# Kernel optimization log

Measured on AMD Instinct MI355X. Metric: run time of the kernel, lower is better.

Reference implementation:

```python
import jax, jax.numpy as jnp
import numpy as np

S, B, E, H, DFF = 1024, 8, 1024, 16, 4096
D = E // H
EPS = 1e-5


def _layernorm(x, g, b):
    m = jnp.mean(x, axis=-1, keepdims=True)
    v = jnp.mean(jnp.square(x - m), axis=-1, keepdims=True)
    return (x - m) * jax.lax.rsqrt(v + EPS) * g + b


def setup_inputs() -> dict:
    key = jax.random.key(0)
    ks = jax.random.split(key, 6)
    return {
        "src": jax.random.normal(ks[0], (S, B, E), jnp.float32),
        "in_proj_w": jax.random.normal(ks[1], (3 * E, E), jnp.float32) * (E ** -0.5),
        "in_proj_b": jnp.zeros((3 * E,), jnp.float32),
        "out_w": jax.random.normal(ks[2], (E, E), jnp.float32) * (E ** -0.5),
        "out_b": jnp.zeros((E,), jnp.float32),
        "ln1_g": jnp.ones((E,), jnp.float32),
        "ln1_b": jnp.zeros((E,), jnp.float32),
        "ln2_g": jnp.ones((E,), jnp.float32),
        "ln2_b": jnp.zeros((E,), jnp.float32),
        "w1": jax.random.normal(ks[3], (DFF, E), jnp.float32) * (E ** -0.5),
        "b1": jnp.zeros((DFF,), jnp.float32),
        "w2": jax.random.normal(ks[4], (E, DFF), jnp.float32) * (DFF ** -0.5),
        "b2": jnp.zeros((E,), jnp.float32),
    }


def reference(src, in_proj_w, in_proj_b, out_w, out_b, ln1_g, ln1_b, ln2_g, ln2_b, w1, b1, w2, b2):
    # src: (S, B, E). Packed in-projection: qkv = src @ W^T + b, split into q,k,v.
    qkv = src @ in_proj_w.T + in_proj_b          # (S, B, 3E)
    q, k, v = jnp.split(qkv, 3, axis=-1)
    q = q.reshape(S, B, H, D)
    k = k.reshape(S, B, H, D)
    v = v.reshape(S, B, H, D)
    # Torch scales q by 1/sqrt(head_dim) before the bmm.
    scores = jnp.einsum("sbhd,tbhd->bhst", q * (D ** -0.5), k)   # (B, H, S, S)
    attn = jax.nn.softmax(scores, axis=-1)
    ctx = jnp.einsum("bhst,tbhd->sbhd", attn, v).reshape(S, B, E)
    attn_out = ctx @ out_w.T + out_b
    # Post-norm encoder layer (norm_first=False), dropout=0.
    x = _layernorm(src + attn_out, ln1_g, ln1_b)
    ff = jax.nn.relu(x @ w1.T + b1) @ w2.T + b2
    return _layernorm(x + ff, ln2_g, ln2_b)
```

## Files before the change

kernel.cpp:

```cpp
#include <hip/hip_runtime.h>

#define S_LEN 1024
#define BATCH 8
#define EMB   1024
#define NH    16
#define HD    64
#define FFD   4096
#define ROWS  (S_LEN*BATCH)

typedef __attribute__((ext_vector_type(8))) short  short8;
typedef __attribute__((ext_vector_type(4))) float  float4v;
typedef __attribute__((ext_vector_type(4))) unsigned int uint4v;

struct alignas(8) us4 { unsigned short x, y, z, w; };

__device__ __forceinline__ unsigned short f2bf(float f) {
    unsigned int u = __float_as_uint(f);
    u += 0x7fffu + ((u >> 16) & 1u);
    return (unsigned short)(u >> 16);
}
__device__ __forceinline__ float bf2f(unsigned short b) {
    return __uint_as_float((unsigned int)b << 16);
}
__device__ __forceinline__ unsigned int cvtpk_bf16(float lo, float hi) {
    unsigned int r;
    asm("v_cvt_pk_bf16_f32 %0, %1, %2" : "=v"(r) : "v"(lo), "v"(hi));
    return r;
}
__device__ __forceinline__ float exp2v(float x) {
    float r;
    asm("v_exp_f32 %0, %1" : "=v"(r) : "v"(x));
    return r;
}

__device__ __forceinline__ void gload_lds16(const void* g, void* l) {
    __builtin_amdgcn_global_load_lds(
        (const __attribute__((address_space(1))) unsigned int*)g,
        (__attribute__((address_space(3))) unsigned int*)l, 16, 0, 0);
}

__device__ __forceinline__ int swz(int row, int chunk) {
    return (row << 7) + ((chunk ^ (row & 7)) << 4);
}

__device__ __forceinline__ void xcd_decode(int id, int& lx, int& ly) {
    int k = id & 7, j = id >> 3;
    ly = k * 4 + (j & 3);
    lx = j >> 2;
}

__global__ __launch_bounds__(256) void cast_bf(const float* __restrict__ in,
                                               unsigned short* __restrict__ out,
                                               int n4) {
    int i = blockIdx.x * 256 + threadIdx.x;
    if (i >= n4) return;
    float4 v = ((const float4*)in)[i];
    us4 o = { f2bf(v.x), f2bf(v.y), f2bf(v.z), f2bf(v.w) };
    ((us4*)out)[i] = o;
}

#define QSCALE 0.18033688011112042f
template <int MODE>
__global__ __launch_bounds__(512, 2) void gemm256(const unsigned short* __restrict__ A,
                                                  const unsigned short* __restrict__ Bw,
                                                  const float* __restrict__ bias,
                                                  unsigned short* __restrict__ outb,
                                                  int M, int N, int K) {
    __shared__ char lds[131072];
    const int tid = threadIdx.x, lane = tid & 63, w = tid >> 6;
    const int wr = w >> 2, wc = w & 3;
    int lx, ly;
    xcd_decode(blockIdx.x, lx, ly);
    const int m0 = ly * 256, n0 = lx * 256;
    const int nt = K >> 6;

    size_t baseA[2], baseB[2];
    int ldsOff[2];
#pragma unroll
    for (int q = 0; q < 2; ++q) {
        int ci = q * 512 + tid;
        int row = ci >> 3;
        int c = (ci & 7) ^ (row & 7);
        baseA[q] = (size_t)(m0 + row) * K + c * 8;
        baseB[q] = (size_t)(n0 + row) * K + c * 8;
        ldsOff[q] = ci * 16;
    }

    auto stage = [&](int kt, int which) {
        int ktc = kt < nt ? kt : 0;
        int slot = kt & 1;
        if (which < 2) {
#pragma unroll
            for (int q = 0; q < 2; ++q)
                gload_lds16(A + baseA[q] + (size_t)which * 128 * K + (size_t)ktc * 64,
                            lds + slot * 32768 + which * 16384 + ldsOff[q]);
        } else {
            int h = which - 2;
#pragma unroll
            for (int q = 0; q < 2; ++q)
                gload_lds16(Bw + baseB[q] + (size_t)h * 128 * K + (size_t)ktc * 64,
                            lds + 65536 + slot * 32768 + h * 16384 + ldsOff[q]);
        }
    };

    auto rdA = [&](int slot, int mh, int i, int mk) -> short8 {
        int arow = wr * 128 + mh * 64 + i * 16 + (lane & 15);
        return *(const short8*)(lds + slot * 32768 + swz(arow, mk * 4 + (lane >> 4)));
    };
    auto rdB = [&](int slot, int nh, int j, int mk) -> short8 {
        int brow = wc * 64 + nh * 32 + j * 16 + (lane & 15);
        return *(const short8*)(lds + 65536 + slot * 32768 + swz(brow, mk * 4 + (lane >> 4)));
    };

    float4v acc[8][4];
#pragma unroll
    for (int i = 0; i < 8; ++i)
#pragma unroll
        for (int j = 0; j < 4; ++j) acc[i][j] = (float4v){0.f, 0.f, 0.f, 0.f};

    short8 a[4][2], b[2][2][2];

    stage(0, 0); stage(0, 1); stage(0, 2); stage(0, 3);
    stage(1, 0);
    asm volatile("s_waitcnt vmcnt(2)" ::: "memory");
    __builtin_amdgcn_s_barrier();

#define MFMA16(MH, NH)                                                          \
    __builtin_amdgcn_s_setprio(1);                                              \
    _Pragma("unroll")                                                           \
    for (int i = 0; i < 4; ++i)                                                 \
        _Pragma("unroll")                                                       \
        for (int j = 0; j < 2; ++j) {                                           \
            acc[(MH)*4+i][(NH)*2+j] = __builtin_amdgcn_mfma_f32_16x16x32_bf16(  \
                a[i][0], b[NH][j][0], acc[(MH)*4+i][(NH)*2+j], 0, 0, 0);        \
            acc[(MH)*4+i][(NH)*2+j] = __builtin_amdgcn_mfma_f32_16x16x32_bf16(  \
                a[i][1], b[NH][j][1], acc[(MH)*4+i][(NH)*2+j], 0, 0, 0);        \
        }                                                                       \
    __builtin_amdgcn_s_setprio(0);

    for (int t = 0; t < nt; ++t) {
        const int slot = t & 1;
#pragma unroll
        for (int i = 0; i < 4; ++i) {
            a[i][0] = rdA(slot, 0, i, 0);
            a[i][1] = rdA(slot, 0, i, 1);
        }
#pragma unroll
        for (int j = 0; j < 2; ++j) {
            b[0][j][0] = rdB(slot, 0, j, 0);
            b[0][j][1] = rdB(slot, 0, j, 1);
        }
        stage(t + 1, 1);
        __builtin_amdgcn_s_barrier();
        asm volatile("s_waitcnt lgkmcnt(0)" ::: "memory");
        __builtin_amdgcn_sched_barrier(0);
        MFMA16(0, 0)
        __builtin_amdgcn_s_barrier();
#pragma unroll
        for (int j = 0; j < 2; ++j) {
            b[1][j][0] = rdB(slot, 1, j, 0);
            b[1][j][1] = rdB(slot, 1, j, 1);
        }
        stage(t + 1, 2);
        __builtin_amdgcn_s_barrier();
        asm volatile("s_waitcnt lgkmcnt(0)" ::: "memory");
        __builtin_amdgcn_sched_barrier(0);
        MFMA16(0, 1)
        __builtin_amdgcn_s_barrier();
#pragma unroll
        for (int i = 0; i < 4; ++i) {
            a[i][0] = rdA(slot, 1, i, 0);
            a[i][1] = rdA(slot, 1, i, 1);
        }
        stage(t + 1, 3);
        __builtin_amdgcn_s_barrier();
        asm volatile("s_waitcnt lgkmcnt(0)" ::: "memory");
        __builtin_amdgcn_sched_barrier(0);
        MFMA16(1, 1)
        __builtin_amdgcn_s_barrier();
        stage(t + 2, 0);
        MFMA16(1, 0)
        asm volatile("s_waitcnt vmcnt(2)" ::: "memory");
        __builtin_amdgcn_s_barrier();
    }
#undef MFMA16
    asm volatile("s_waitcnt vmcnt(0)" ::: "memory");

#pragma unroll
    for (int mi = 0; mi < 8; ++mi) {
#pragma unroll
        for (int nj = 0; nj < 4; ++nj) {
            int col = n0 + wc * 64 + nj * 16 + (lane & 15);
            float bv = bias[col];
#pragma unroll
            for (int r = 0; r < 4; ++r) {
                int row = m0 + wr * 128 + mi * 16 + (lane >> 4) * 4 + r;
                size_t idx = (size_t)row * N + col;
                float v = acc[mi][nj][r] + bv;
                if (MODE == 0) {
                    if (col < EMB) v *= QSCALE;
                    outb[idx] = f2bf(v);
                } else {
                    outb[idx] = f2bf(fmaxf(v, 0.f));
                }
            }
        }
    }
}

template <int MODE>
__global__ __launch_bounds__(512, 2) void gemm256n(const unsigned short* __restrict__ A,
                                                   const unsigned short* __restrict__ Bw,
                                                   const float* __restrict__ bias,
                                                   const float* __restrict__ res,
                                                   const unsigned short* __restrict__ resb,
                                                   float* __restrict__ outf,
                                                   int M, int N, int K) {
    __shared__ char lds[98304];
    const int tid = threadIdx.x, lane = tid & 63, w = tid >> 6;
    const int wr = w >> 1, wc = w & 1;
    int lx, ly;
    xcd_decode(blockIdx.x, lx, ly);
    const int m0 = ly * 256, n0 = lx * 128;
    const int nt = K >> 6;
    const int g = lane >> 4, qs = lane & 15;

    size_t baseA[4], baseB[2];
    int ldsOffA[4], ldsOffB[2];
#pragma unroll
    for (int q = 0; q < 4; ++q) {
        int ci = q * 512 + tid;
        int row = ci >> 3;
        int c = (ci & 7) ^ (row & 7);
        baseA[q] = (size_t)(m0 + row) * K + c * 8;
        ldsOffA[q] = ci * 16;
    }
#pragma unroll
    for (int q = 0; q < 2; ++q) {
        int ci = q * 512 + tid;
        int row = ci >> 3;
        int c = (ci & 7) ^ (row & 7);
        baseB[q] = (size_t)(n0 + row) * K + c * 8;
        ldsOffB[q] = ci * 16;
    }

    auto stage = [&](int kt, int which) {
        int ktc = kt < nt ? kt : 0;
        int slot = kt & 1;
        if (which < 2) {
#pragma unroll
            for (int q = 0; q < 2; ++q) {
                int qq = which * 2 + q;
                gload_lds16(A + baseA[qq] + (size_t)ktc * 64,
                            lds + slot * 32768 + ldsOffA[qq]);
            }
        } else {
#pragma unroll
            for (int q = 0; q < 2; ++q)
                gload_lds16(Bw + baseB[q] + (size_t)ktc * 64,
                            lds + 65536 + slot * 16384 + ldsOffB[q]);
        }
    };

    auto rdA = [&](int slot, int i, int mk) -> short8 {
        int arow = wr * 64 + i * 16 + qs;
        return *(const short8*)(lds + slot * 32768 + swz(arow, mk * 4 + g));
    };
    auto rdB = [&](int slot, int j, int mk) -> short8 {
        int brow = wc * 64 + j * 16 + qs;
        return *(const short8*)(lds + 65536 + slot * 16384 + swz(brow, mk * 4 + g));
    };

    float4v acc[4][4];
#pragma unroll
    for (int i = 0; i < 4; ++i)
#pragma unroll
        for (int j = 0; j < 4; ++j) acc[i][j] = (float4v){0.f, 0.f, 0.f, 0.f};

    short8 a[4][2], b[4][2];

    stage(0, 0); stage(0, 1); stage(0, 2);
    stage(1, 0);
    asm volatile("s_waitcnt vmcnt(2)" ::: "memory");
    __builtin_amdgcn_s_barrier();

    for (int t = 0; t < nt; ++t) {
        const int slot = t & 1;
#pragma unroll
        for (int i = 0; i < 4; ++i) {
            a[i][0] = rdA(slot, i, 0);
            a[i][1] = rdA(slot, i, 1);
        }
#pragma unroll
        for (int j = 0; j < 2; ++j) {
            b[j][0] = rdB(slot, j, 0);
            b[j][1] = rdB(slot, j, 1);
        }
        stage(t + 1, 1);
        __builtin_amdgcn_s_barrier();
        asm volatile("s_waitcnt lgkmcnt(0)" ::: "memory");
        __builtin_amdgcn_sched_barrier(0);
        __builtin_amdgcn_s_setprio(1);
#pragma unroll
        for (int i = 0; i < 4; ++i)
#pragma unroll
            for (int j = 0; j < 2; ++j) {
                acc[i][j] = __builtin_amdgcn_mfma_f32_16x16x32_bf16(
                    a[i][0], b[j][0], acc[i][j], 0, 0, 0);
                acc[i][j] = __builtin_amdgcn_mfma_f32_16x16x32_bf16(
                    a[i][1], b[j][1], acc[i][j], 0, 0, 0);
            }
        __builtin_amdgcn_s_setprio(0);
        __builtin_amdgcn_s_barrier();
#pragma unroll
        for (int j = 2; j < 4; ++j) {
            b[j][0] = rdB(slot, j, 0);
            b[j][1] = rdB(slot, j, 1);
        }
        stage(t + 1, 2);
        __builtin_amdgcn_s_barrier();
        asm volatile("s_waitcnt lgkmcnt(0)" ::: "memory");
        __builtin_amdgcn_sched_barrier(0);
        __builtin_amdgcn_s_setprio(1);
#pragma unroll
        for (int i = 0; i < 4; ++i)
#pragma unroll
            for (int j = 2; j < 4; ++j)
                acc[i][j] = __builtin_amdgcn_mfma_f32_16x16x32_bf16(
                    a[i][0], b[j][0], acc[i][j], 0, 0, 0);
        __builtin_amdgcn_s_setprio(0);
        __builtin_amdgcn_s_barrier();
        stage(t + 2, 0);
        __builtin_amdgcn_s_setprio(1);
#pragma unroll
        for (int i = 0; i < 4; ++i)
#pragma unroll
            for (int j = 2; j < 4; ++j)
                acc[i][j] = __builtin_amdgcn_mfma_f32_16x16x32_bf16(
                    a[i][1], b[j][1], acc[i][j], 0, 0, 0);
        __builtin_amdgcn_s_setprio(0);
        asm volatile("s_waitcnt vmcnt(2)" ::: "memory");
        __builtin_amdgcn_s_barrier();
    }
    asm volatile("s_waitcnt vmcnt(0)" ::: "memory");

#pragma unroll
    for (int mi = 0; mi < 4; ++mi) {
#pragma unroll
        for (int j = 0; j < 4; ++j) {
            int col = n0 + wc * 64 + j * 16 + qs;
            float bv = bias[col];
#pragma unroll
            for (int r = 0; r < 4; ++r) {
                int row = m0 + wr * 64 + mi * 16 + g * 4 + r;
                size_t idx = (size_t)row * N + col;
                float v = acc[mi][j][r] + bv;
                if (MODE == 1) outf[idx] = v + res[idx];
                else           outf[idx] = v + bf2f(resb[idx]);
            }
        }
    }
}

__global__ __launch_bounds__(256) void vtrans(const unsigned short* __restrict__ qkv,
                                              unsigned short* __restrict__ vt) {
    const int bh = blockIdx.y, b = bh >> 4, h = bh & 15;
    const int t0 = blockIdx.x * 64;
    const int tid = threadIdx.x;
    __shared__ unsigned short lds[64][72];
#pragma unroll
    for (int rep = 0; rep < 2; ++rep) {
        int slot = rep * 256 + tid;
        int row = slot >> 3, cc = slot & 7;
        const unsigned short* g =
            qkv + ((size_t)(t0 + row) * BATCH + b) * 3072 + 2 * EMB + h * 64 + cc * 8;
        *(uint4v*)&lds[row][cc * 8] = *(const uint4v*)g;
    }
    __syncthreads();
#pragma unroll
    for (int rep = 0; rep < 2; ++rep) {
        int slot = rep * 256 + tid;
        int d = slot >> 3, tc = slot & 7;
        unsigned short tmp[8] __attribute__((aligned(16)));
#pragma unroll
        for (int j = 0; j < 8; ++j) tmp[j] = lds[tc * 8 + j][d];
        unsigned short* g = vt + ((size_t)bh * 64 + d) * S_LEN + t0 + tc * 8;
        *(uint4v*)g = *(const uint4v*)tmp;
    }
}

__global__ __launch_bounds__(256, 6) void attn(const unsigned short* __restrict__ qkv,
                                               const unsigned short* __restrict__ vt,
                                               unsigned short* __restrict__ ctx) {
    __shared__ char Ks[64 * 128];
    __shared__ char Vs[64 * 128];
    __shared__ char QP[64 * 128];
    const int tid = threadIdx.x, lane = tid & 63, w = tid >> 6;
    const int bh = blockIdx.x & 127, b = bh >> 4, h = bh & 15;
    const int s0 = (blockIdx.x >> 7) * 64;
    const int g = lane >> 4, qs = lane & 15;

#pragma unroll
    for (int p = 0; p < 2; ++p) {
        int ci = p * 256 + tid;
        int row = ci >> 3, c = (ci & 7) ^ (row & 7);
        gload_lds16(qkv + ((size_t)(s0 + row) * BATCH + b) * 3072 + h * 64 + c * 8,
                    QP + (p * 256 + w * 64) * 16);
    }
    __syncthreads();

    short8 qa0 = *(const short8*)(QP + swz(w * 16 + qs, 0 * 4 + g));
    short8 qa1 = *(const short8*)(QP + swz(w * 16 + qs, 1 * 4 + g));
    asm volatile("s_waitcnt lgkmcnt(0)" ::: "memory");
    __builtin_amdgcn_sched_barrier(0);
    char* Ps = QP + w * 2048;

    float4v O[4];
#pragma unroll
    for (int df = 0; df < 4; ++df) O[df] = (float4v){0.f, 0.f, 0.f, 0.f};
    float m_s = -1e30f;
    float l_s = 0.f;

    for (int t0 = 0; t0 < S_LEN; t0 += 64) {
        __syncthreads();
#pragma unroll
        for (int p = 0; p < 2; ++p) {
            int ci = p * 256 + tid;
            int row = ci >> 3, c = (ci & 7) ^ (row & 7);
            gload_lds16(qkv + ((size_t)(t0 + row) * BATCH + b) * 3072 + EMB + h * 64 + c * 8,
                        Ks + (p * 256 + w * 64) * 16);
            gload_lds16(vt + ((size_t)bh * 64 + row) * S_LEN + t0 + c * 8,
                        Vs + (p * 256 + w * 64) * 16);
        }
        __syncthreads();

        float4v Sf[4];
#pragma unroll
        for (int tf = 0; tf < 4; ++tf) Sf[tf] = (float4v){0.f, 0.f, 0.f, 0.f};
#pragma unroll
        for (int tf = 0; tf < 4; ++tf) {
            int kr = tf * 16 + qs;
            short8 kb0 = *(const short8*)(Ks + swz(kr, 0 * 4 + g));
            short8 kb1 = *(const short8*)(Ks + swz(kr, 1 * 4 + g));
            Sf[tf] = __builtin_amdgcn_mfma_f32_16x16x32_bf16(kb0, qa0, Sf[tf], 0, 0, 0);
            Sf[tf] = __builtin_amdgcn_mfma_f32_16x16x32_bf16(kb1, qa1, Sf[tf], 0, 0, 0);
        }

        float mx = fmaxf(fmaxf(Sf[0][0], Sf[0][1]), fmaxf(Sf[0][2], Sf[0][3]));
#pragma unroll
        for (int tf = 1; tf < 4; ++tf)
            mx = fmaxf(mx, fmaxf(fmaxf(Sf[tf][0], Sf[tf][1]),
                                 fmaxf(Sf[tf][2], Sf[tf][3])));
        mx = fmaxf(mx, __shfl_xor(mx, 16));
        mx = fmaxf(mx, __shfl_xor(mx, 32));

        if (!__all(mx - m_s <= 8.0f)) {
            float mnew = fmaxf(m_s, mx);
            float alpha = exp2v(m_s - mnew);
            m_s = mnew;
            l_s *= alpha;
#pragma unroll
            for (int r = 0; r < 4; ++r) {
                float ar = __shfl(alpha, 4 * g + r);
#pragma unroll
                for (int df = 0; df < 4; ++df) O[df][r] *= ar;
            }
        }

        float rs = 0.f;
#pragma unroll
        for (int tf = 0; tf < 4; ++tf) {
            float p0 = exp2v(Sf[tf][0] - m_s);
            float p1 = exp2v(Sf[tf][1] - m_s);
            float p2 = exp2v(Sf[tf][2] - m_s);
            float p3 = exp2v(Sf[tf][3] - m_s);
            rs += (p0 + p1) + (p2 + p3);
            uint2 pk = make_uint2(cvtpk_bf16(p0, p1), cvtpk_bf16(p2, p3));
            *(uint2*)(Ps + (qs << 7) +
                      (((2 * tf + (g >> 1)) ^ (qs & 7)) << 4) + ((g & 1) << 3)) = pk;
        }
        rs += __shfl_xor(rs, 16);
        rs += __shfl_xor(rs, 32);
        l_s += rs;

        asm volatile("s_waitcnt lgkmcnt(0)" ::: "memory");
        __builtin_amdgcn_sched_barrier(0);

#pragma unroll
        for (int mk = 0; mk < 2; ++mk) {
            short8 pa = *(const short8*)(Ps + swz(qs, mk * 4 + g));
#pragma unroll
            for (int df = 0; df < 4; ++df) {
                int vr = df * 16 + qs;
                short8 vb = *(const short8*)(Vs + swz(vr, mk * 4 + g));
                O[df] = __builtin_amdgcn_mfma_f32_16x16x32_bf16(pa, vb, O[df], 0, 0, 0);
            }
        }
    }

    float inv = __builtin_amdgcn_rcpf(l_s);
#pragma unroll
    for (int r = 0; r < 4; ++r) {
        float ir = __shfl(inv, 4 * g + r);
#pragma unroll
        for (int df = 0; df < 4; ++df) {
            int srow = s0 + w * 16 + g * 4 + r;
            int d    = df * 16 + qs;
            ctx[((size_t)srow * BATCH + b) * EMB + h * 64 + d] = f2bf(O[df][r] * ir);
        }
    }
}

__global__ __launch_bounds__(256) void ln_ker(const float* __restrict__ y,
                                              const float* __restrict__ g,
                                              const float* __restrict__ bta,
                                              float* __restrict__ xo,
                                              unsigned short* __restrict__ xb) {
    const int row = blockIdx.x, tid = threadIdx.x, lane = tid & 63, w = tid >> 6;
    float4 v = ((const float4*)(y + (size_t)row * EMB))[tid];
    float s = v.x + v.y + v.z + v.w;
    float q = v.x * v.x + v.y * v.y + v.z * v.z + v.w * v.w;
#pragma unroll
    for (int m = 1; m < 64; m <<= 1) {
        s += __shfl_xor(s, m);
        q += __shfl_xor(q, m);
    }
    __shared__ float ps[4], pq[4];
    if (lane == 0) { ps[w] = s; pq[w] = q; }
    __syncthreads();
    s = ps[0] + ps[1] + ps[2] + ps[3];
    q = pq[0] + pq[1] + pq[2] + pq[3];
    float mean = s * (1.f / EMB);
    float var  = q * (1.f / EMB) - mean * mean;
    float rstd = rsqrtf(var + 1e-5f);
    float4 gv = ((const float4*)g)[tid];
    float4 bv = ((const float4*)bta)[tid];
    float4 o;
    o.x = (v.x - mean) * rstd * gv.x + bv.x;
    o.y = (v.y - mean) * rstd * gv.y + bv.y;
    o.z = (v.z - mean) * rstd * gv.z + bv.z;
    o.w = (v.w - mean) * rstd * gv.w + bv.w;
    if (xo) ((float4*)(xo + (size_t)row * EMB))[tid] = o;
    if (xb) {
        us4 ob = { f2bf(o.x), f2bf(o.y), f2bf(o.z), f2bf(o.w) };
        ((us4*)(xb + (size_t)row * EMB))[tid] = ob;
    }
}

extern "C" void kernel_launch(void* const* d_in, const int* in_sizes, int n_in,
                              void* d_out, int out_size, void* d_ws, size_t ws_size,
                              hipStream_t stream) {
    (void)in_sizes; (void)n_in; (void)out_size;
    const float* src       = (const float*)d_in[0];
    const float* in_proj_w = (const float*)d_in[1];
    const float* in_proj_b = (const float*)d_in[2];
    const float* out_w     = (const float*)d_in[3];
    const float* out_b     = (const float*)d_in[4];
    const float* ln1_g     = (const float*)d_in[5];
    const float* ln1_b     = (const float*)d_in[6];
    const float* ln2_g     = (const float*)d_in[7];
    const float* ln2_b     = (const float*)d_in[8];
    const float* w1        = (const float*)d_in[9];
    const float* b1        = (const float*)d_in[10];
    const float* w2        = (const float*)d_in[11];
    const float* b2        = (const float*)d_in[12];

    const size_t MB = 1u << 20;
    if (ws_size < 104 * MB) return;

    char* ws = (char*)d_ws;
    unsigned short* wqkvb = (unsigned short*)(ws);
    unsigned short* wob   = (unsigned short*)(ws + 6 * MB);
    unsigned short* w1b   = (unsigned short*)(ws + 8 * MB);
    unsigned short* w2b   = (unsigned short*)(ws + 16 * MB);
    unsigned short* qkvb  = (unsigned short*)(ws + 24 * MB);
    unsigned short* srcbf = (unsigned short*)(ws + 72 * MB);
    unsigned short* vtb   = (unsigned short*)(ws + 88 * MB);
    unsigned short* ctxb  = (unsigned short*)(ws + 72 * MB);
    unsigned short* xbf   = (unsigned short*)(ws + 24 * MB);
    unsigned short* hb    = (unsigned short*)(ws + 40 * MB);
    float*          yout  = (float*)d_out;

    auto castn = [&](const float* in, unsigned short* out, size_t n) {
        int n4 = (int)(n / 4);
        cast_bf<<<(n4 + 255) / 256, 256, 0, stream>>>(in, out, n4);
    };
    castn(src, srcbf, (size_t)ROWS * EMB);
    castn(in_proj_w, wqkvb, (size_t)3 * EMB * EMB);
    castn(out_w, wob, (size_t)EMB * EMB);
    castn(w1, w1b, (size_t)FFD * EMB);
    castn(w2, w2b, (size_t)EMB * FFD);

    gemm256<0><<<(3 * EMB / 256) * 32, 512, 0, stream>>>(
        srcbf, wqkvb, in_proj_b, qkvb, ROWS, 3 * EMB, EMB);

    vtrans<<<dim3(S_LEN / 64, BATCH * NH), 256, 0, stream>>>(qkvb, vtb);

    attn<<<(S_LEN / 64) * BATCH * NH, 256, 0, stream>>>(qkvb, vtb, ctxb);

    gemm256n<1><<<(EMB / 128) * 32, 512, 0, stream>>>(
        ctxb, wob, out_b, src, nullptr, yout, ROWS, EMB, EMB);

    ln_ker<<<ROWS, 256, 0, stream>>>(yout, ln1_g, ln1_b, nullptr, xbf);

    gemm256<2><<<(FFD / 256) * 32, 512, 0, stream>>>(
        xbf, w1b, b1, hb, ROWS, FFD, EMB);

    gemm256n<3><<<(EMB / 128) * 32, 512, 0, stream>>>(
        hb, w2b, b2, nullptr, xbf, yout, ROWS, EMB, FFD);

    ln_ker<<<ROWS, 256, 0, stream>>>(yout, ln2_g, ln2_b, (float*)d_out, nullptr);
}
```

Baseline: 340.3 us.

## Triple-buffer LDS in residual GEMM and collapse per-iteration barrier phases

Replaces the double-buffered, three-phase staged main loop of the residual-fused GEMM with a three-slot LDS ring. Each iteration prefetches the full A and B tiles two steps ahead, loads all fragments, and runs all MFMAs between a single wait and barrier. The goal is to drop most of the per-iteration barriers and hide global-load latency with a deeper prefetch. In exchange, LDS use grows to 144 KB per block, which rules out running a second block on a CU, and the interleaving of loads with compute becomes coarser.

```diff
diff --git a/kernel.cpp b/kernel.cpp
--- a/kernel.cpp
+++ b/kernel.cpp
@@ -216,7 +216,7 @@
                                                    const unsigned short* __restrict__ resb,
                                                    float* __restrict__ outf,
                                                    int M, int N, int K) {
-    __shared__ char lds[98304];
+    __shared__ char lds[147456];
     const int tid = threadIdx.x, lane = tid & 63, w = tid >> 6;
     const int wr = w >> 1, wc = w & 1;
     int lx, ly;
@@ -244,22 +244,17 @@
         ldsOffB[q] = ci * 16;
     }
 
-    auto stage = [&](int kt, int which) {
+    auto stage = [&](int kt) {
         int ktc = kt < nt ? kt : 0;
-        int slot = kt & 1;
-        if (which < 2) {
-#pragma unroll
-            for (int q = 0; q < 2; ++q) {
-                int qq = which * 2 + q;
-                gload_lds16(A + baseA[qq] + (size_t)ktc * 64,
-                            lds + slot * 32768 + ldsOffA[qq]);
-            }
-        } else {
-#pragma unroll
-            for (int q = 0; q < 2; ++q)
-                gload_lds16(Bw + baseB[q] + (size_t)ktc * 64,
-                            lds + 65536 + slot * 16384 + ldsOffB[q]);
-        }
+        int slot = kt % 3;
+#pragma unroll
+        for (int q = 0; q < 4; ++q)
+            gload_lds16(A + baseA[q] + (size_t)ktc * 64,
+                        lds + slot * 32768 + ldsOffA[q]);
+#pragma unroll
+        for (int q = 0; q < 2; ++q)
+            gload_lds16(Bw + baseB[q] + (size_t)ktc * 64,
+                        lds + 98304 + slot * 16384 + ldsOffB[q]);
     };
 
     auto rdA = [&](int slot, int i, int mk) -> short8 {
@@ -268,7 +263,7 @@
     };
     auto rdB = [&](int slot, int j, int mk) -> short8 {
         int brow = wc * 64 + j * 16 + qs;
-        return *(const short8*)(lds + 65536 + slot * 16384 + swz(brow, mk * 4 + g));
+        return *(const short8*)(lds + 98304 + slot * 16384 + swz(brow, mk * 4 + g));
     };
 
     float4v acc[4][4];
@@ -279,67 +274,37 @@
 
     short8 a[4][2], b[4][2];
 
-    stage(0, 0); stage(0, 1); stage(0, 2);
-    stage(1, 0);
-    asm volatile("s_waitcnt vmcnt(2)" ::: "memory");
+    stage(0); stage(1);
+    asm volatile("s_waitcnt vmcnt(6)" ::: "memory");
     __builtin_amdgcn_s_barrier();
 
     for (int t = 0; t < nt; ++t) {
-        const int slot = t & 1;
+        const int slot = t % 3;
 #pragma unroll
         for (int i = 0; i < 4; ++i) {
             a[i][0] = rdA(slot, i, 0);
             a[i][1] = rdA(slot, i, 1);
         }
 #pragma unroll
-        for (int j = 0; j < 2; ++j) {
+        for (int j = 0; j < 4; ++j) {
             b[j][0] = rdB(slot, j, 0);
             b[j][1] = rdB(slot, j, 1);
         }
-        stage(t + 1, 1);
-        __builtin_amdgcn_s_barrier();
+        stage(t + 2);
         asm volatile("s_waitcnt lgkmcnt(0)" ::: "memory");
         __builtin_amdgcn_sched_barrier(0);
         __builtin_amdgcn_s_setprio(1);
 #pragma unroll
         for (int i = 0; i < 4; ++i)
 #pragma unroll
-            for (int j = 0; j < 2; ++j) {
+            for (int j = 0; j < 4; ++j) {
                 acc[i][j] = __builtin_amdgcn_mfma_f32_16x16x32_bf16(
                     a[i][0], b[j][0], acc[i][j], 0, 0, 0);
                 acc[i][j] = __builtin_amdgcn_mfma_f32_16x16x32_bf16(
                     a[i][1], b[j][1], acc[i][j], 0, 0, 0);
             }
         __builtin_amdgcn_s_setprio(0);
-        __builtin_amdgcn_s_barrier();
-#pragma unroll
-        for (int j = 2; j < 4; ++j) {
-            b[j][0] = rdB(slot, j, 0);
-            b[j][1] = rdB(slot, j, 1);
-        }
-        stage(t + 1, 2);
-        __builtin_amdgcn_s_barrier();
-        asm volatile("s_waitcnt lgkmcnt(0)" ::: "memory");
-        __builtin_amdgcn_sched_barrier(0);
-        __builtin_amdgcn_s_setprio(1);
-#pragma unroll
-        for (int i = 0; i < 4; ++i)
-#pragma unroll
-            for (int j = 2; j < 4; ++j)
-                acc[i][j] = __builtin_amdgcn_mfma_f32_16x16x32_bf16(
-                    a[i][0], b[j][0], acc[i][j], 0, 0, 0);
-        __builtin_amdgcn_s_setprio(0);
-        __builtin_amdgcn_s_barrier();
-        stage(t + 2, 0);
-        __builtin_amdgcn_s_setprio(1);
-#pragma unroll
-        for (int i = 0; i < 4; ++i)
-#pragma unroll
-            for (int j = 2; j < 4; ++j)
-                acc[i][j] = __builtin_amdgcn_mfma_f32_16x16x32_bf16(
-                    a[i][1], b[j][1], acc[i][j], 0, 0, 0);
-        __builtin_amdgcn_s_setprio(0);
-        asm volatile("s_waitcnt vmcnt(2)" ::: "memory");
+        asm volatile("s_waitcnt vmcnt(6)" ::: "memory");
         __builtin_amdgcn_s_barrier();
     }
     asm volatile("s_waitcnt vmcnt(0)" ::: "memory");
```

Result: faster. 331.9 us (-2.5%).
